# Kernel tuning notes

Measured on AMD Instinct MI355X. Metric: run time of the kernel, lower is better.

## Reference

```python
import jax, jax.numpy as jnp
import numpy as np

D = 2048      # hidden dim
H = 16        # heads
BSZ = 4       # batch
L = 2048      # seq len
BASE_DT = 0.1


def setup_inputs() -> dict:
    key = jax.random.key(0)
    ks = jax.random.split(key, 9)
    s = 1.0 / np.sqrt(D)
    x = jax.random.normal(ks[0], (BSZ, L, D), dtype=jnp.float32)
    v = jax.random.normal(ks[1], (BSZ, L, D), dtype=jnp.float32)
    force = jax.random.normal(ks[2], (BSZ, L, D), dtype=jnp.float32)
    WA = jax.random.normal(ks[3], (D, D), dtype=jnp.float32) * s
    bA = jnp.zeros((D,), dtype=jnp.float32)
    WB = jax.random.normal(ks[4], (D, D), dtype=jnp.float32) * s
    bB = jnp.zeros((D,), dtype=jnp.float32)
    Wdt = jax.random.normal(ks[5], (D, D), dtype=jnp.float32) * s
    bdt = jnp.zeros((D,), dtype=jnp.float32)
    # base_dt_scales buffer: 1.5**head_index, repeated head_dim times
    scales = jnp.repeat(1.5 ** jnp.arange(H, dtype=jnp.float32), D // H)
    return {"x": x, "v": v, "force": force, "WA": WA, "bA": bA,
            "WB": WB, "bB": bB, "Wdt": Wdt, "bdt": bdt, "scales": scales}


def _combine(e1, e2):
    # associative op for v_t = a_t * v_{t-1} + b_t ; e1 is the earlier element
    a1, b1 = e1
    a2, b2 = e2
    return a1 * a2, a2 * b1 + b2


def reference(x, v, force, WA, bA, WB, bB, Wdt, bdt, scales):
    # x is LayerNorm-ed in the original but the result is unused; v is unused.
    A = jax.nn.sigmoid(force @ WA + bA)                      # [B, L, D] in (0,1)
    dt = jax.nn.softplus(force @ Wdt + bdt) * BASE_DT * scales  # per-head dt scaling
    B_val = (force @ WB + bB) * dt
    # parallel associative scan over the sequence axis: v_t = A_t v_{t-1} + B_t
    _, v_seq = jax.lax.associative_scan(_combine, (A, B_val), axis=1)
    # second scan has A=1 -> plain prefix sum
    x_seq = jnp.cumsum(v_seq * dt, axis=1)
    return x_seq, v_seq
```

## Files before the change

### kernel.cpp

```cpp
#include <hip/hip_runtime.h>
#include <hip/hip_bf16.h>
#include <cstdint>
#include <cstddef>

#define D_DIM 2048
#define L_SEQ 2048
#define B_SZ 4
#define M_ROWS (B_SZ * L_SEQ)
#define NT_COLS (3 * D_DIM)
#define NCH 16
#define CHUNK (L_SEQ / NCH)

typedef __bf16 bf16_t;
typedef bf16_t bf16x4 __attribute__((ext_vector_type(4)));
typedef bf16_t bf16x8 __attribute__((ext_vector_type(8)));
typedef float f32x4 __attribute__((ext_vector_type(4)));

__device__ __forceinline__ void gl_lds16(const void* g, void* l) {
    __builtin_amdgcn_global_load_lds(
        (const __attribute__((address_space(1))) unsigned int*)g,
        (__attribute__((address_space(3))) unsigned int*)l, 16, 0, 0);
}

__global__ __launch_bounds__(256) void cvt_bf16_kernel(
    const float* __restrict__ in, bf16_t* __restrict__ out, int n4)
{
    int i = blockIdx.x * 256 + threadIdx.x;
    if (i >= n4) return;
    float4 f = ((const float4*)in)[i];
    bf16x4 o;
    o[0] = (bf16_t)f.x; o[1] = (bf16_t)f.y; o[2] = (bf16_t)f.z; o[3] = (bf16_t)f.w;
    ((bf16x4*)out)[i] = o;
}

__global__ __launch_bounds__(256) void transpose_w_kernel(
    const float* __restrict__ W, bf16_t* __restrict__ Wt)
{
    __shared__ float tile[32][33];
    int j0 = blockIdx.x * 32, k0 = blockIdx.y * 32;
    int tx = threadIdx.x, ty = threadIdx.y;
#pragma unroll
    for (int i = 0; i < 4; i++) {
        int k = k0 + ty + i * 8;
        tile[ty + i * 8][tx] = W[(size_t)k * D_DIM + j0 + tx];
    }
    __syncthreads();
#pragma unroll
    for (int i = 0; i < 4; i++) {
        int j = j0 + ty + i * 8;
        Wt[(size_t)j * D_DIM + k0 + tx] = (bf16_t)tile[tx][ty + i * 8];
    }
}

__global__ __launch_bounds__(256) void gemm_fused_kernel(
    const bf16_t* __restrict__ Abf,
    const bf16_t* __restrict__ Wt,
    const float* __restrict__ bA, const float* __restrict__ bdt,
    const float* __restrict__ bB, const float* __restrict__ scales,
    float* __restrict__ outA,
    float* __restrict__ outDT,
    float* __restrict__ outB)
{
    __shared__ bf16_t lds_a[128 * 32];
    __shared__ bf16_t lds_b[128 * 32];

    const int bm0 = blockIdx.x * 128;
    const int bn0 = blockIdx.y * 128;
    const int t = threadIdx.x;
    const int lane = t & 63, w = t >> 6;
    const int wr = (w >> 1) * 64;
    const int wc = (w & 1) * 64;

    f32x4 acc[4][4] = {};

    const int lin0 = t, lin1 = t + 256;
    const int ar0 = lin0 >> 2, ac0 = (lin0 & 3) * 8;
    const int ar1 = lin1 >> 2, ac1 = (lin1 & 3) * 8;
    const int frow = lane & 15;
    const int fk = (lane >> 4) * 8;

    for (int k0 = 0; k0 < D_DIM; k0 += 32) {
        gl_lds16(Abf + (size_t)(bm0 + ar0) * D_DIM + k0 + ac0, lds_a + w * 512);
        gl_lds16(Abf + (size_t)(bm0 + ar1) * D_DIM + k0 + ac1, lds_a + 2048 + w * 512);
        gl_lds16(Wt  + (size_t)(bn0 + ar0) * D_DIM + k0 + ac0, lds_b + w * 512);
        gl_lds16(Wt  + (size_t)(bn0 + ar1) * D_DIM + k0 + ac1, lds_b + 2048 + w * 512);
        __syncthreads();

        bf16x8 af[4], bfr[4];
#pragma unroll
        for (int m = 0; m < 4; m++)
            af[m] = *(const bf16x8*)&lds_a[(wr + m * 16 + frow) * 32 + fk];
#pragma unroll
        for (int n = 0; n < 4; n++)
            bfr[n] = *(const bf16x8*)&lds_b[(wc + n * 16 + frow) * 32 + fk];
#pragma unroll
        for (int m = 0; m < 4; m++)
#pragma unroll
            for (int n = 0; n < 4; n++)
                acc[m][n] = __builtin_amdgcn_mfma_f32_16x16x32_bf16(
                    af[m], bfr[n], acc[m][n], 0, 0, 0);
        __syncthreads();
    }

    const int seg = bn0 >> 11;
    const int dbase = (bn0 & 2047) + wc + (lane & 15);
    const int rowbase = bm0 + wr + ((lane >> 4) << 2);
#pragma unroll
    for (int m = 0; m < 4; m++) {
#pragma unroll
        for (int n = 0; n < 4; n++) {
            int d = dbase + n * 16;
#pragma unroll
            for (int r = 0; r < 4; r++) {
                int gm = rowbase + m * 16 + r;
                size_t idx = (size_t)gm * D_DIM + d;
                float val = acc[m][n][r];
                if (seg == 0) {
                    outA[idx] = 1.0f / (1.0f + __expf(-(val + bA[d])));
                } else if (seg == 1) {
                    float xx = val + bdt[d];
                    float sp = xx > 0.f ? xx + log1pf(__expf(-xx)) : log1pf(__expf(xx));
                    outDT[idx] = sp * 0.1f * scales[d];
                } else {
                    outB[idx] = val + bB[d];
                }
            }
        }
    }
}

__global__ __launch_bounds__(256) void scan_pass1_kernel(
    const float* __restrict__ Aarr, const float* __restrict__ Braw,
    const float* __restrict__ dtarr, float4* __restrict__ agg)
{
    int tid = blockIdx.x * 256 + threadIdx.x;
    int d = tid & (D_DIM - 1);
    int c = (tid >> 11) & (NCH - 1);
    int b = tid >> 15;
    size_t base = ((size_t)b * L_SEQ + c * CHUNK) * D_DIM + d;
    float P = 1.f, R = 0.f, U = 0.f, Wg = 0.f;
#pragma unroll 4
    for (int tt = 0; tt < CHUNK; tt++) {
        size_t idx = base + (size_t)tt * D_DIM;
        float a = Aarr[idx], rb = Braw[idx], dt = dtarr[idx];
        float bv = rb * dt;
        float da = dt * a;
        R = da * P + R;
        Wg = da * U + dt * bv + Wg;
        U = a * U + bv;
        P = a * P;
    }
    agg[tid] = make_float4(P, R, U, Wg);
}

__global__ __launch_bounds__(256) void scan_pass2_kernel(
    const float4* __restrict__ agg, float2* __restrict__ pre)
{
    int tid = blockIdx.x * 256 + threadIdx.x;
    int d = tid & (D_DIM - 1);
    int b = tid >> 11;
    float v = 0.f, x = 0.f;
#pragma unroll
    for (int c = 0; c < NCH; c++) {
        int i = ((b * NCH + c) << 11) + d;
        float4 g = agg[i];
        pre[i] = make_float2(v, x);
        float vn = g.x * v + g.z;
        x = g.y * v + x + g.w;
        v = vn;
    }
}

__global__ __launch_bounds__(256) void scan_pass3_kernel(
    const float* __restrict__ dtarr, const float2* __restrict__ pre,
    float* __restrict__ xout ,
    float* __restrict__ vout )
{
    int tid = blockIdx.x * 256 + threadIdx.x;
    int d = tid & (D_DIM - 1);
    int c = (tid >> 11) & (NCH - 1);
    int b = tid >> 15;
    float2 s = pre[((b * NCH + c) << 11) + d];
    float v = s.x, x = s.y;
    size_t base = ((size_t)b * L_SEQ + c * CHUNK) * D_DIM + d;
#pragma unroll 4
    for (int tt = 0; tt < CHUNK; tt++) {
        size_t idx = base + (size_t)tt * D_DIM;
        float a = xout[idx];
        float rb = vout[idx];
        float dt = dtarr[idx];
        v = a * v + rb * dt;
        x = x + v * dt;
        vout[idx] = v;
        xout[idx] = x;
    }
}

extern "C" void kernel_launch(void* const* d_in, const int* in_sizes, int n_in,
                              void* d_out, int out_size, void* d_ws, size_t ws_size,
                              hipStream_t stream) {
    const float* force  = (const float*)d_in[2];
    const float* WA     = (const float*)d_in[3];
    const float* bA     = (const float*)d_in[4];
    const float* WB     = (const float*)d_in[5];
    const float* bB     = (const float*)d_in[6];
    const float* Wdt    = (const float*)d_in[7];
    const float* bdt    = (const float*)d_in[8];
    const float* scales = (const float*)d_in[9];

    float* xout = (float*)d_out;
    float* vout = xout + (size_t)M_ROWS * D_DIM;

    char* ws = (char*)d_ws;
    bf16_t* fbf = (bf16_t*)ws;
    bf16_t* wt  = (bf16_t*)(ws + (size_t)33554432);
    float*  dtv = (float*)(ws + (size_t)33554432 + 25165824);
    float4* agg = (float4*)(ws + (size_t)33554432 + 25165824 + 67108864);
    float2* pre = (float2*)(ws + (size_t)33554432 + 25165824 + 67108864 + 2097152);

    {
        int n4 = M_ROWS * D_DIM / 4;
        cvt_bf16_kernel<<<n4 / 256, 256, 0, stream>>>(force, fbf, n4);
    }
    {
        dim3 grid(D_DIM / 32, D_DIM / 32), block(32, 8);
        transpose_w_kernel<<<grid, block, 0, stream>>>(WA,  wt);
        transpose_w_kernel<<<grid, block, 0, stream>>>(Wdt, wt + (size_t)D_DIM * D_DIM);
        transpose_w_kernel<<<grid, block, 0, stream>>>(WB,  wt + (size_t)2 * D_DIM * D_DIM);
    }
    {
        dim3 grid(M_ROWS / 128, NT_COLS / 128);
        gemm_fused_kernel<<<grid, 256, 0, stream>>>(fbf, wt, bA, bdt, bB, scales,
                                                    xout, dtv, vout);
    }
    scan_pass1_kernel<<<(B_SZ * NCH * D_DIM) / 256, 256, 0, stream>>>(xout, vout, dtv, agg);
    scan_pass2_kernel<<<(B_SZ * D_DIM) / 256, 256, 0, stream>>>(agg, pre);
    scan_pass3_kernel<<<(B_SZ * NCH * D_DIM) / 256, 256, 0, stream>>>(dtv, pre, xout, vout);
}
```

Baseline: 498.6 us.

## Swizzle GEMM LDS layout, remap blocks per XCD, merge transposes, widen bf16 convert

XOR-swizzles the GEMM's LDS tile layout to cut bank conflicts on fragment reads. Remaps the flat block index so each XCD handles a fixed group of N-column tiles, aiming for better L2 reuse of weights. It also merges the three weight-transpose launches into one 3D grid and makes the bf16 conversion handle 8 elements per thread. A leftover duplicate loop of A-fragment loads is overwritten right away and should be removed by the compiler, so it is harmless.

```diff
diff --git a/kernel.cpp b/kernel.cpp
--- a/kernel.cpp
+++ b/kernel.cpp
@@ -23,20 +23,25 @@
 }
 
 __global__ __launch_bounds__(256) void cvt_bf16_kernel(
-    const float* __restrict__ in, bf16_t* __restrict__ out, int n4)
+    const float* __restrict__ in, bf16_t* __restrict__ out, int n8)
 {
     int i = blockIdx.x * 256 + threadIdx.x;
-    if (i >= n4) return;
-    float4 f = ((const float4*)in)[i];
-    bf16x4 o;
-    o[0] = (bf16_t)f.x; o[1] = (bf16_t)f.y; o[2] = (bf16_t)f.z; o[3] = (bf16_t)f.w;
-    ((bf16x4*)out)[i] = o;
+    if (i >= n8) return;
+    float4 f0 = ((const float4*)in)[2 * i];
+    float4 f1 = ((const float4*)in)[2 * i + 1];
+    bf16x8 o;
+    o[0] = (bf16_t)f0.x; o[1] = (bf16_t)f0.y; o[2] = (bf16_t)f0.z; o[3] = (bf16_t)f0.w;
+    o[4] = (bf16_t)f1.x; o[5] = (bf16_t)f1.y; o[6] = (bf16_t)f1.z; o[7] = (bf16_t)f1.w;
+    ((bf16x8*)out)[i] = o;
 }
 
 __global__ __launch_bounds__(256) void transpose_w_kernel(
-    const float* __restrict__ W, bf16_t* __restrict__ Wt)
+    const float* __restrict__ W0, const float* __restrict__ W1,
+    const float* __restrict__ W2, bf16_t* __restrict__ Wt)
 {
     __shared__ float tile[32][33];
+    const float* W = (blockIdx.z == 0) ? W0 : (blockIdx.z == 1) ? W1 : W2;
+    bf16_t* dst = Wt + (size_t)blockIdx.z * D_DIM * D_DIM;
     int j0 = blockIdx.x * 32, k0 = blockIdx.y * 32;
     int tx = threadIdx.x, ty = threadIdx.y;
 #pragma unroll
@@ -48,7 +53,7 @@
 #pragma unroll
     for (int i = 0; i < 4; i++) {
         int j = j0 + ty + i * 8;
-        Wt[(size_t)j * D_DIM + k0 + tx] = (bf16_t)tile[tx][ty + i * 8];
+        dst[(size_t)j * D_DIM + k0 + tx] = (bf16_t)tile[tx][ty + i * 8];
     }
 }
 
@@ -64,8 +69,12 @@
     __shared__ bf16_t lds_a[128 * 32];
     __shared__ bf16_t lds_b[128 * 32];
 
-    const int bm0 = blockIdx.x * 128;
-    const int bn0 = blockIdx.y * 128;
+    const int bid = blockIdx.x;
+    const int xcd = bid & 7;
+    const int local = bid >> 3;
+    const int bm0 = (local / 6) * 128;
+    const int bn0 = (xcd * 6 + (local % 6)) * 128;
+
     const int t = threadIdx.x;
     const int lane = t & 63, w = t >> 6;
     const int wr = (w >> 1) * 64;
@@ -73,26 +82,29 @@
 
     f32x4 acc[4][4] = {};
 
-    const int lin0 = t, lin1 = t + 256;
-    const int ar0 = lin0 >> 2, ac0 = (lin0 & 3) * 8;
-    const int ar1 = lin1 >> 2, ac1 = (lin1 & 3) * 8;
+    const int ar0 = t >> 2;
+    const int ac0 = (((t & 3) ^ ((t >> 3) & 3)) << 3);
     const int frow = lane & 15;
-    const int fk = (lane >> 4) * 8;
+    const int loff = frow * 32 + (((lane >> 4) ^ ((frow >> 1) & 3)) << 3);
 
     for (int k0 = 0; k0 < D_DIM; k0 += 32) {
         gl_lds16(Abf + (size_t)(bm0 + ar0) * D_DIM + k0 + ac0, lds_a + w * 512);
-        gl_lds16(Abf + (size_t)(bm0 + ar1) * D_DIM + k0 + ac1, lds_a + 2048 + w * 512);
+        gl_lds16(Abf + (size_t)(bm0 + ar0 + 64) * D_DIM + k0 + ac0, lds_a + 2048 + w * 512);
         gl_lds16(Wt  + (size_t)(bn0 + ar0) * D_DIM + k0 + ac0, lds_b + w * 512);
-        gl_lds16(Wt  + (size_t)(bn0 + ar1) * D_DIM + k0 + ac1, lds_b + 2048 + w * 512);
+        gl_lds16(Wt  + (size_t)(bn0 + ar0 + 64) * D_DIM + k0 + ac0, lds_b + 2048 + w * 512);
         __syncthreads();
 
         bf16x8 af[4], bfr[4];
 #pragma unroll
         for (int m = 0; m < 4; m++)
-            af[m] = *(const bf16x8*)&lds_a[(wr + m * 16 + frow) * 32 + fk];
+            af[m] = *(const bf16x8*)&lds_a[(wr + m * 16 + frow) * 32 + (loff - frow * 32)]
+                ;
+#pragma unroll
+        for (int m = 0; m < 4; m++)
+            af[m] = *(const bf16x8*)&lds_a[(wr + m * 16) * 32 + loff];
 #pragma unroll
         for (int n = 0; n < 4; n++)
-            bfr[n] = *(const bf16x8*)&lds_b[(wc + n * 16 + frow) * 32 + fk];
+            bfr[n] = *(const bf16x8*)&lds_b[(wc + n * 16) * 32 + loff];
 #pragma unroll
         for (int m = 0; m < 4; m++)
 #pragma unroll
@@ -173,8 +185,7 @@
 
 __global__ __launch_bounds__(256) void scan_pass3_kernel(
     const float* __restrict__ dtarr, const float2* __restrict__ pre,
-    float* __restrict__ xout ,
-    float* __restrict__ vout )
+    float* __restrict__ xout, float* __restrict__ vout)
 {
     int tid = blockIdx.x * 256 + threadIdx.x;
     int d = tid & (D_DIM - 1);
@@ -219,17 +230,15 @@
     float2* pre = (float2*)(ws + (size_t)33554432 + 25165824 + 67108864 + 2097152);
 
     {
-        int n4 = M_ROWS * D_DIM / 4;
-        cvt_bf16_kernel<<<n4 / 256, 256, 0, stream>>>(force, fbf, n4);
+        int n8 = M_ROWS * D_DIM / 8;
+        cvt_bf16_kernel<<<n8 / 256, 256, 0, stream>>>(force, fbf, n8);
     }
     {
-        dim3 grid(D_DIM / 32, D_DIM / 32), block(32, 8);
-        transpose_w_kernel<<<grid, block, 0, stream>>>(WA,  wt);
-        transpose_w_kernel<<<grid, block, 0, stream>>>(Wdt, wt + (size_t)D_DIM * D_DIM);
-        transpose_w_kernel<<<grid, block, 0, stream>>>(WB,  wt + (size_t)2 * D_DIM * D_DIM);
+        dim3 grid(D_DIM / 32, D_DIM / 32, 3), block(32, 8);
+        transpose_w_kernel<<<grid, block, 0, stream>>>(WA, Wdt, WB, wt);
     }
     {
-        dim3 grid(M_ROWS / 128, NT_COLS / 128);
+        dim3 grid((M_ROWS / 128) * (NT_COLS / 128));
         gemm_fused_kernel<<<grid, 256, 0, stream>>>(fbf, wt, bA, bdt, bB, scales,
                                                     xout, dtv, vout);
     }
```

New measurement: 622.1 us. 1.25x slower.
